# Kernel optimization log

Hardware: AMD Instinct MI355X
Metric: run time of the kernel (lower is better)

Reference implementation:

```python
import jax, jax.numpy as jnp
import numpy as np

B, S, HID = 2, 2048, 2048
H, KVH, D = 32, 8, 64          # query heads, kv heads, head_dim
G = H // KVH                    # GQA group size (num_key_value_groups)
ROT = 32                        # head_dim * partial_rotary_factor
THETA = 10000.0
NEG = -1e9


def setup_inputs() -> dict:
    key = jax.random.key(0)
    ks = jax.random.split(key, 5)
    hidden_states = jax.random.normal(ks[0], (B, S, HID), jnp.float32) * 0.02
    Wq = jax.random.normal(ks[1], (H * D, HID), jnp.float32) * 0.02
    Wk = jax.random.normal(ks[2], (KVH * D, HID), jnp.float32) * 0.02
    Wv = jax.random.normal(ks[3], (KVH * D, HID), jnp.float32) * 0.02
    Wo = jax.random.normal(ks[4], (HID, H * D), jnp.float32) * 0.02
    # rotary embeddings over the partial rotary dims
    inv_freq = 1.0 / (THETA ** (jnp.arange(0, ROT, 2, dtype=jnp.float32) / ROT))
    freqs = jnp.arange(S, dtype=jnp.float32)[:, None] * inv_freq[None, :]  # [S, ROT/2]
    emb = jnp.concatenate([freqs, freqs], axis=-1)                         # [S, ROT]
    cos = jnp.broadcast_to(jnp.cos(emb)[None], (B, S, ROT)).astype(jnp.float32)
    sin = jnp.broadcast_to(jnp.sin(emb)[None], (B, S, ROT)).astype(jnp.float32)
    # HF-style additive causal mask [1, 1, S, S]
    causal = jnp.tril(jnp.ones((S, S), dtype=bool))
    attention_mask = jnp.where(causal, 0.0, NEG).astype(jnp.float32)[None, None]
    return {"hidden_states": hidden_states, "cos": cos, "sin": sin,
            "attention_mask": attention_mask, "Wq": Wq, "Wk": Wk, "Wv": Wv, "Wo": Wo}


def _rotate_half(x):
    half = x.shape[-1] // 2
    return jnp.concatenate([-x[..., half:], x[..., :half]], axis=-1)


def _apply_partial_rope(x, cos, sin):
    # x: [B, h, S, D]; cos/sin: [B, 1, S, ROT]
    xr, xp = x[..., :ROT], x[..., ROT:]
    xr = xr * cos + _rotate_half(xr) * sin
    return jnp.concatenate([xr, xp], axis=-1)


def reference(hidden_states, cos, sin, attention_mask, Wq, Wk, Wv, Wo):
    bsz, q_len, _ = hidden_states.shape
    q = (hidden_states @ Wq.T).reshape(bsz, q_len, H, D).transpose(0, 2, 1, 3)    # [B,H,S,D]
    k = (hidden_states @ Wk.T).reshape(bsz, q_len, KVH, D).transpose(0, 2, 1, 3)  # [B,KVH,S,D]
    v = (hidden_states @ Wv.T).reshape(bsz, q_len, KVH, D).transpose(0, 2, 1, 3)
    cos_e, sin_e = cos[:, None], sin[:, None]  # unsqueeze_dim=1
    q = _apply_partial_rope(q, cos_e, sin_e)
    k = _apply_partial_rope(k, cos_e, sin_e)
    # GQA: group q heads instead of materializing repeat_kv (same math)
    qg = q.reshape(bsz, KVH, G, q_len, D)
    scores = jnp.einsum('bkgsd,bktd->bkgst', qg, k) / jnp.sqrt(jnp.float32(D))
    scores = scores + attention_mask[:, :, None, :, :q_len]  # [B,KVH,G,S,S]
    attn = jax.nn.softmax(scores.astype(jnp.float32), axis=-1).astype(q.dtype)
    out = jnp.einsum('bkgst,bktd->bkgsd', attn, v)
    out = out.reshape(bsz, H, q_len, D).transpose(0, 2, 1, 3).reshape(bsz, q_len, H * D)
    return out @ Wo.T
```

## Files before the change

kernel.cpp:

```cpp
#include <hip/hip_runtime.h>
#include <hip/hip_bf16.h>

#define BATCH 2
#define SEQ 2048
#define HID 2048
#define NH 32
#define NKVH 8
#define HD 64
#define GQ 4
#define ROT 32

typedef __attribute__((ext_vector_type(8))) short bf16x8;
typedef __attribute__((ext_vector_type(8))) unsigned short u16x8;
typedef __attribute__((ext_vector_type(4))) float f32x4;
typedef unsigned int u32;
typedef unsigned short u16;

#define MFMA_BF16(A, B, C) __builtin_amdgcn_mfma_f32_16x16x32_bf16(A, B, C, 0, 0, 0)

#define QSCALE 0.180336880111120f

__device__ __forceinline__ void gload_lds16(const void* g, void* l) {
    __builtin_amdgcn_global_load_lds(
        (const __attribute__((address_space(1))) unsigned int*)g,
        (__attribute__((address_space(3))) unsigned int*)l, 16, 0, 0);
}

__device__ __forceinline__ u16 f2b(float x) {
    union { __hip_bfloat16 h; u16 u; } cv;
    cv.h = __float2bfloat16(x);
    return cv.u;
}
__device__ __forceinline__ u32 pack2r(float lo, float hi) {
    u32 a = __builtin_bit_cast(u32, lo) + 0x8000u;
    u32 b = __builtin_bit_cast(u32, hi) + 0x8000u;
    return __builtin_amdgcn_perm(b, a, 0x07060302u);
}

__global__ __launch_bounds__(256) void cast_all(
    const float* __restrict__ hs, const float* __restrict__ Wq,
    const float* __restrict__ Wk, const float* __restrict__ Wv,
    const float* __restrict__ Wo, u16* __restrict__ d_hs, u16* __restrict__ d_Wq,
    u16* __restrict__ d_Wk, u16* __restrict__ d_Wv, u16* __restrict__ d_Wo) {
    const int bx = blockIdx.x;
    const float* s;
    u16* d;
    int off;
    if (bx < 4096) { s = hs; d = d_hs; off = bx; }
    else if (bx < 6144) { s = Wq; d = d_Wq; off = bx - 4096; }
    else if (bx < 6656) { s = Wk; d = d_Wk; off = bx - 6144; }
    else if (bx < 7168) { s = Wv; d = d_Wv; off = bx - 6656; }
    else { s = Wo; d = d_Wo; off = bx - 7168; }
    const size_t i = (size_t)off * 2048 + threadIdx.x * 8;
    const float4 a = *(const float4*)&s[i];
    const float4 b = *(const float4*)&s[i + 4];
    u16x8 v;
    v[0] = f2b(a.x); v[1] = f2b(a.y); v[2] = f2b(a.z); v[3] = f2b(a.w);
    v[4] = f2b(b.x); v[5] = f2b(b.y); v[6] = f2b(b.z); v[7] = f2b(b.w);
    *(u16x8*)&d[i] = v;
}

__global__ __launch_bounds__(256) void qkv_gemm(
    const u16* __restrict__ A, const u16* __restrict__ Wq,
    const u16* __restrict__ Wk, const u16* __restrict__ Wv,
    u16* __restrict__ Qb, u16* __restrict__ Kb, u16* __restrict__ Vt,
    const float* __restrict__ cosp, const float* __restrict__ sinp) {
    const int x = blockIdx.x;
    int mode, n0;
    const u16* __restrict__ W;
    if (x < 16)      { mode = 0; W = Wq; n0 = x * 128; }
    else if (x < 20) { mode = 1; W = Wk; n0 = (x - 16) * 128; }
    else             { mode = 2; W = Wv; n0 = (x - 20) * 128; }

    __shared__ __align__(16) u16 As[128 * 32];
    __shared__ __align__(16) u16 Ws[128 * 32];
    const int tid = threadIdx.x;
    const int lane = tid & 63, wave = tid >> 6;
    const int ar = lane & 15, quad = lane >> 4;
    const int m0 = blockIdx.y * 128;
    const int wm = (wave >> 1) * 64, wn = (wave & 1) * 64;

    f32x4 acc[4][4] = {};

    for (int k0 = 0; k0 < HID; k0 += 32) {
#pragma unroll
        for (int it = 0; it < 2; ++it) {
            const int ci = it * 256 + tid;
            const int row = ci >> 2, kcl = ci & 3;
            const int kcg = kcl ^ ((row >> 1) & 3);
            gload_lds16(&A[(size_t)(m0 + row) * HID + k0 + kcg * 8], &As[ci * 8]);
            gload_lds16(&W[(size_t)(n0 + row) * HID + k0 + kcg * 8], &Ws[ci * 8]);
        }
        __syncthreads();
        bf16x8 af[4], bf[4];
#pragma unroll
        for (int t = 0; t < 4; ++t) {
            const int ra = wm + t * 16 + ar;
            af[t] = *(const bf16x8*)&As[ra * 32 + (quad ^ ((ra >> 1) & 3)) * 8];
            const int rb = wn + t * 16 + ar;
            bf[t] = *(const bf16x8*)&Ws[rb * 32 + (quad ^ ((rb >> 1) & 3)) * 8];
        }
#pragma unroll
        for (int mt = 0; mt < 4; ++mt)
#pragma unroll
            for (int nt = 0; nt < 4; ++nt)
                acc[mt][nt] = MFMA_BF16(af[mt], bf[nt], acc[mt][nt]);
        __syncthreads();
    }

    if (mode < 2) {
        const float SC = (mode == 0) ? QSCALE : 1.0f;
        u16* __restrict__ C = (mode == 0) ? Qb : Kb;
        const int N = (mode == 0) ? 2048 : 512;
#pragma unroll
        for (int mt = 0; mt < 4; ++mt) {
            const int r0 = m0 + wm + mt * 16 + quad * 4;
#pragma unroll
            for (int r = 0; r < 4; ++r) {
                const int t = r0 + r;
                const float* cp = &cosp[(size_t)t * ROT];
                const float* sp = &sinp[(size_t)t * ROT];
                const float c0 = cp[ar], s0 = sp[ar];
                const float c1 = cp[ar + 16], s1 = sp[ar + 16];
                const float x0 = acc[mt][0][r], x1 = acc[mt][1][r];
                u16* crow = &C[(size_t)t * N + n0 + wn];
                crow[ar]      = f2b((x0 * c0 - x1 * s0) * SC);
                crow[ar + 16] = f2b((x1 * c1 + x0 * s1) * SC);
                crow[ar + 32] = f2b(acc[mt][2][r] * SC);
                crow[ar + 48] = f2b(acc[mt][3][r] * SC);
            }
        }
    } else {
#pragma unroll
        for (int mt = 0; mt < 4; ++mt) {
            const int r0 = m0 + wm + mt * 16 + quad * 4;
            const int bb = r0 >> 11;
            const int s = r0 & 2047;
            const int ca = (s >> 2) & 7;
            const int cl = ((ca & 3) << 1) | (ca >> 2);
            const int spos = (s & ~31) + cl * 4;
#pragma unroll
            for (int nt = 0; nt < 4; ++nt) {
                const int c = n0 + wn + nt * 16 + ar;
                const int kvh = c >> 6, d = c & 63;
                ushort4 v;
                v.x = f2b(acc[mt][nt][0]); v.y = f2b(acc[mt][nt][1]);
                v.z = f2b(acc[mt][nt][2]); v.w = f2b(acc[mt][nt][3]);
                *(ushort4*)&Vt[((size_t)(bb * NKVH + kvh) * HD + d) * SEQ + spos] = v;
            }
        }
    }
}

__global__ __launch_bounds__(256) void gemm_bt(const u16* __restrict__ A,
                                               const u16* __restrict__ W,
                                               float* __restrict__ C,
                                               int M, int N, int K) {
    __shared__ __align__(16) u16 As[128 * 32];
    __shared__ __align__(16) u16 Ws[128 * 32];
    const int tid = threadIdx.x;
    const int lane = tid & 63, wave = tid >> 6;
    const int ar = lane & 15, quad = lane >> 4;
    const int m0 = blockIdx.y * 128, n0 = blockIdx.x * 128;
    const int wm = (wave >> 1) * 64, wn = (wave & 1) * 64;

    f32x4 acc[4][4] = {};

    for (int k0 = 0; k0 < K; k0 += 32) {
#pragma unroll
        for (int it = 0; it < 2; ++it) {
            const int ci = it * 256 + tid;
            const int row = ci >> 2, kcl = ci & 3;
            const int kcg = kcl ^ ((row >> 1) & 3);
            gload_lds16(&A[(size_t)(m0 + row) * K + k0 + kcg * 8], &As[ci * 8]);
            gload_lds16(&W[(size_t)(n0 + row) * K + k0 + kcg * 8], &Ws[ci * 8]);
        }
        __syncthreads();
        bf16x8 af[4], bf[4];
#pragma unroll
        for (int t = 0; t < 4; ++t) {
            const int ra = wm + t * 16 + ar;
            af[t] = *(const bf16x8*)&As[ra * 32 + (quad ^ ((ra >> 1) & 3)) * 8];
            const int rb = wn + t * 16 + ar;
            bf[t] = *(const bf16x8*)&Ws[rb * 32 + (quad ^ ((rb >> 1) & 3)) * 8];
        }
#pragma unroll
        for (int mt = 0; mt < 4; ++mt)
#pragma unroll
            for (int nt = 0; nt < 4; ++nt)
                acc[mt][nt] = MFMA_BF16(af[mt], bf[nt], acc[mt][nt]);
        __syncthreads();
    }

#pragma unroll
    for (int mt = 0; mt < 4; ++mt) {
        const int r0 = m0 + wm + mt * 16 + quad * 4;
#pragma unroll
        for (int nt = 0; nt < 4; ++nt) {
            const int c = n0 + wn + nt * 16 + ar;
#pragma unroll
            for (int r = 0; r < 4; ++r)
                C[(size_t)(r0 + r) * N + c] = acc[mt][nt][r];
        }
    }
}

__global__ __launch_bounds__(256, 2) void flash_attn_mfma(
    const u16* __restrict__ Qg, const u16* __restrict__ Kg,
    const u16* __restrict__ Vtg, u16* __restrict__ AO) {
    const int p = blockIdx.x, h = blockIdx.y, b = blockIdx.z;
    const int kvh = h / GQ;
    const int tid = threadIdx.x;
    const int lane = tid & 63, w = tid >> 6;
    const int n = lane & 15, quad = lane >> 4;

    __shared__ __align__(16) u16 Qs[128 * 64];
    __shared__ __align__(16) u16 Ks[2 * 64 * 64];
    __shared__ __align__(16) u16 Vts[2 * 64 * 64];

    for (int ph = 0; ph < 2; ++ph) {
        const int bq = ph ? (15 - p) : p;
        const int q0 = bq * 128;

#pragma unroll
        for (int it = 0; it < 4; ++it) {
            const int ci = it * 256 + tid;
            const int row = ci >> 3, kcg = (ci & 7) ^ (row & 7);
            gload_lds16(&Qg[(size_t)((b * SEQ + q0 + row) * NH + h) * HD + kcg * 8],
                        &Qs[ci * 8]);
        }
#pragma unroll
        for (int it = 0; it < 2; ++it) {
            const int ci = it * 256 + tid;
            const int row = ci >> 3, kcg = (ci & 7) ^ (row & 7);
            gload_lds16(&Kg[(size_t)((b * SEQ + row) * NKVH + kvh) * HD + kcg * 8],
                        &Ks[ci * 8]);
            gload_lds16(&Vtg[(size_t)((b * NKVH + kvh) * HD + row) * SEQ + kcg * 8],
                        &Vts[ci * 8]);
        }
        __syncthreads();

        bf16x8 Qf[2][2];
#pragma unroll
        for (int t = 0; t < 2; ++t)
#pragma unroll
            for (int kh = 0; kh < 2; ++kh) {
                const int qrow = w * 32 + t * 16 + n;
                const int c = (kh * 4 + quad) ^ (qrow & 7);
                Qf[t][kh] = *(const bf16x8*)&Qs[qrow * 64 + c * 8];
            }

        f32x4 O[2][4] = {};
        float lsum[2] = {0.f, 0.f};

        const int ktmax = 2 * bq + 1;
        for (int kt = 0; kt <= ktmax; ++kt) {
            const int cur = kt & 1;
            if (kt < ktmax) {
                const int base = (cur ^ 1) * 4096;
#pragma unroll
                for (int it = 0; it < 2; ++it) {
                    const int ci = it * 256 + tid;
                    const int row = ci >> 3, kcg = (ci & 7) ^ (row & 7);
                    gload_lds16(&Kg[(size_t)((b * SEQ + (kt + 1) * 64 + row) * NKVH + kvh) * HD + kcg * 8],
                                &Ks[base + ci * 8]);
                    gload_lds16(&Vtg[(size_t)((b * NKVH + kvh) * HD + row) * SEQ + (kt + 1) * 64 + kcg * 8],
                                &Vts[base + ci * 8]);
                }
            }
            const u16* Kl = &Ks[cur * 4096];
            const u16* Vl = &Vts[cur * 4096];

            f32x4 sc[2][4] = {};
#pragma unroll
            for (int kh = 0; kh < 2; ++kh)
#pragma unroll
                for (int k4 = 0; k4 < 4; ++k4) {
                    const int krow = k4 * 16 + n;
                    const int c = (kh * 4 + quad) ^ (krow & 7);
                    const bf16x8 Kf = *(const bf16x8*)&Kl[krow * 64 + c * 8];
                    sc[0][k4] = MFMA_BF16(Kf, Qf[0][kh], sc[0][k4]);
                    sc[1][k4] = MFMA_BF16(Kf, Qf[1][kh], sc[1][k4]);
                }

            const bool masked = (kt >= 2 * bq);
            bf16x8 Pf[2][2];
#pragma unroll
            for (int t = 0; t < 2; ++t) {
                const int qg = q0 + w * 32 + t * 16 + n;
                if (masked) {
#pragma unroll
                    for (int k4 = 0; k4 < 4; ++k4)
#pragma unroll
                        for (int r = 0; r < 4; ++r)
                            if (kt * 64 + k4 * 16 + quad * 4 + r > qg)
                                sc[t][k4][r] = -1e30f;
                }
                float sk[4];
#pragma unroll
                for (int k4 = 0; k4 < 4; ++k4) {
                    const float e0 = exp2f(sc[t][k4][0]);
                    const float e1 = exp2f(sc[t][k4][1]);
                    const float e2 = exp2f(sc[t][k4][2]);
                    const float e3 = exp2f(sc[t][k4][3]);
                    sc[t][k4][0] = e0; sc[t][k4][1] = e1;
                    sc[t][k4][2] = e2; sc[t][k4][3] = e3;
                    sk[k4] = (e0 + e1) + (e2 + e3);
                }
                lsum[t] += (sk[0] + sk[1]) + (sk[2] + sk[3]);
#pragma unroll
                for (int kb = 0; kb < 2; ++kb) {
                    union { u32 uw[4]; bf16x8 v; } cv;
#pragma unroll
                    for (int a = 0; a < 2; ++a) {
                        cv.uw[a * 2 + 0] = pack2r(sc[t][2 * kb + a][0], sc[t][2 * kb + a][1]);
                        cv.uw[a * 2 + 1] = pack2r(sc[t][2 * kb + a][2], sc[t][2 * kb + a][3]);
                    }
                    Pf[t][kb] = cv.v;
                }
            }

#pragma unroll
            for (int kb = 0; kb < 2; ++kb)
#pragma unroll
                for (int dt = 0; dt < 4; ++dt) {
                    const int drow = dt * 16 + n;
                    const int c = (kb * 4 + quad) ^ (drow & 7);
                    const bf16x8 Vf = *(const bf16x8*)&Vl[drow * 64 + c * 8];
                    O[0][dt] = MFMA_BF16(Vf, Pf[0][kb], O[0][dt]);
                    O[1][dt] = MFMA_BF16(Vf, Pf[1][kb], O[1][dt]);
                }
            __syncthreads();
        }

#pragma unroll
        for (int t = 0; t < 2; ++t) {
            float rs = lsum[t];
            rs += __shfl_xor(rs, 16, 64);
            rs += __shfl_xor(rs, 32, 64);
            const int qg = q0 + w * 32 + t * 16 + n;
            const float inv = 1.f / rs;
#pragma unroll
            for (int dt = 0; dt < 4; ++dt) {
                u32 v2[2];
                v2[0] = pack2r(O[t][dt][0] * inv, O[t][dt][1] * inv);
                v2[1] = pack2r(O[t][dt][2] * inv, O[t][dt][3] * inv);
                *(u32*)&AO[(size_t)((b * SEQ + qg) * NH + h) * HD + dt * 16 + quad * 4] = v2[0];
                *(u32*)&AO[(size_t)((b * SEQ + qg) * NH + h) * HD + dt * 16 + quad * 4 + 2] = v2[1];
            }
        }
    }
}

extern "C" void kernel_launch(void* const* d_in, const int* in_sizes, int n_in,
                              void* d_out, int out_size, void* d_ws,
                              size_t ws_size, hipStream_t stream) {
    const float* hs = (const float*)d_in[0];
    const float* cosp = (const float*)d_in[1];
    const float* sinp = (const float*)d_in[2];
    const float* Wq = (const float*)d_in[4];
    const float* Wk = (const float*)d_in[5];
    const float* Wv = (const float*)d_in[6];
    const float* Wo = (const float*)d_in[7];
    float* out = (float*)d_out;

    u16* ws = (u16*)d_ws;
    u16* hs_bf = ws;
    u16* Wq_bf = hs_bf + (size_t)4096 * 2048;
    u16* Wk_bf = Wq_bf + (size_t)2048 * 2048;
    u16* Wv_bf = Wk_bf + (size_t)512 * 2048;
    u16* Wo_bf = Wv_bf + (size_t)512 * 2048;
    u16* Qb = Wo_bf + (size_t)2048 * 2048;
    u16* Kb = Qb + (size_t)4096 * 2048;
    u16* Vt = Kb + (size_t)4096 * 512;
    u16* AO = hs_bf;

    cast_all<<<dim3(9216), 256, 0, stream>>>(hs, Wq, Wk, Wv, Wo, hs_bf, Wq_bf,
                                             Wk_bf, Wv_bf, Wo_bf);

    qkv_gemm<<<dim3(24, 32), 256, 0, stream>>>(hs_bf, Wq_bf, Wk_bf, Wv_bf, Qb,
                                               Kb, Vt, cosp, sinp);

    flash_attn_mfma<<<dim3(8, NH, BATCH), 256, 0, stream>>>(Qb, Kb, Vt, AO);

    gemm_bt<<<dim3(16, 32), 256, 0, stream>>>(AO, Wo_bf, out, 4096, 2048, 2048);
}
```

Baseline: 337.6 us.

## Remap GEMM blocks per XCD and transpose MFMA operands for vectorized epilogue stores

Both GEMM kernels now use a 1D grid whose block index is remapped so that the blocks sharing a weight column-tile land on the same XCD, aiming to improve L2 reuse of weight tiles. The MFMA operands are swapped for the Q/K and output GEMMs so each lane holds four consecutive columns, which lets the epilogues use packed 8-byte and 16-byte stores and float4 cos/sin loads instead of scalar stores. The V path and the attention output store also switch to packed uint2 writes. The mapping depends on the round-robin assignment of blocks to XCDs and on grid sizes that divide evenly.

```diff
diff --git a/kernel.cpp b/kernel.cpp
--- a/kernel.cpp
+++ b/kernel.cpp
@@ -65,7 +65,11 @@
     const u16* __restrict__ Wk, const u16* __restrict__ Wv,
     u16* __restrict__ Qb, u16* __restrict__ Kb, u16* __restrict__ Vt,
     const float* __restrict__ cosp, const float* __restrict__ sinp) {
-    const int x = blockIdx.x;
+    const int bid = blockIdx.x;
+    const int xcd = bid & 7, loc = bid >> 3;
+    const int x = xcd * 3 + (loc % 3);
+    const int m0 = (loc / 3) * 128;
+
     int mode, n0;
     const u16* __restrict__ W;
     if (x < 16)      { mode = 0; W = Wq; n0 = x * 128; }
@@ -77,7 +81,7 @@
     const int tid = threadIdx.x;
     const int lane = tid & 63, wave = tid >> 6;
     const int ar = lane & 15, quad = lane >> 4;
-    const int m0 = blockIdx.y * 128;
+    const int q4 = quad * 4;
     const int wm = (wave >> 1) * 64, wn = (wave & 1) * 64;
 
     f32x4 acc[4][4] = {};
@@ -100,11 +104,19 @@
             const int rb = wn + t * 16 + ar;
             bf[t] = *(const bf16x8*)&Ws[rb * 32 + (quad ^ ((rb >> 1) & 3)) * 8];
         }
-#pragma unroll
-        for (int mt = 0; mt < 4; ++mt)
-#pragma unroll
-            for (int nt = 0; nt < 4; ++nt)
-                acc[mt][nt] = MFMA_BF16(af[mt], bf[nt], acc[mt][nt]);
+        if (mode < 2) {
+#pragma unroll
+            for (int mt = 0; mt < 4; ++mt)
+#pragma unroll
+                for (int nt = 0; nt < 4; ++nt)
+                    acc[mt][nt] = MFMA_BF16(bf[nt], af[mt], acc[mt][nt]);
+        } else {
+#pragma unroll
+            for (int mt = 0; mt < 4; ++mt)
+#pragma unroll
+                for (int nt = 0; nt < 4; ++nt)
+                    acc[mt][nt] = MFMA_BF16(af[mt], bf[nt], acc[mt][nt]);
+        }
         __syncthreads();
     }
 
@@ -114,26 +126,39 @@
         const int N = (mode == 0) ? 2048 : 512;
 #pragma unroll
         for (int mt = 0; mt < 4; ++mt) {
-            const int r0 = m0 + wm + mt * 16 + quad * 4;
+            const int t = m0 + wm + mt * 16 + ar;
+            const float4 c0 = *(const float4*)&cosp[(size_t)t * ROT + q4];
+            const float4 s0 = *(const float4*)&sinp[(size_t)t * ROT + q4];
+            const float4 c1 = *(const float4*)&cosp[(size_t)t * ROT + 16 + q4];
+            const float4 s1 = *(const float4*)&sinp[(size_t)t * ROT + 16 + q4];
+            u16* crow = &C[(size_t)t * N + n0 + wn];
+            const f32x4 x0 = acc[mt][0], x1 = acc[mt][1];
+            const float cr0[4] = {c0.x, c0.y, c0.z, c0.w};
+            const float sr0[4] = {s0.x, s0.y, s0.z, s0.w};
+            const float cr1[4] = {c1.x, c1.y, c1.z, c1.w};
+            const float sr1[4] = {s1.x, s1.y, s1.z, s1.w};
+            float o0[4], o1[4];
 #pragma unroll
             for (int r = 0; r < 4; ++r) {
-                const int t = r0 + r;
-                const float* cp = &cosp[(size_t)t * ROT];
-                const float* sp = &sinp[(size_t)t * ROT];
-                const float c0 = cp[ar], s0 = sp[ar];
-                const float c1 = cp[ar + 16], s1 = sp[ar + 16];
-                const float x0 = acc[mt][0][r], x1 = acc[mt][1][r];
-                u16* crow = &C[(size_t)t * N + n0 + wn];
-                crow[ar]      = f2b((x0 * c0 - x1 * s0) * SC);
-                crow[ar + 16] = f2b((x1 * c1 + x0 * s1) * SC);
-                crow[ar + 32] = f2b(acc[mt][2][r] * SC);
-                crow[ar + 48] = f2b(acc[mt][3][r] * SC);
-            }
+                o0[r] = (x0[r] * cr0[r] - x1[r] * sr0[r]) * SC;
+                o1[r] = (x1[r] * cr1[r] + x0[r] * sr1[r]) * SC;
+            }
+            uint2 v;
+            v.x = pack2r(o0[0], o0[1]); v.y = pack2r(o0[2], o0[3]);
+            *(uint2*)&crow[q4] = v;
+            v.x = pack2r(o1[0], o1[1]); v.y = pack2r(o1[2], o1[3]);
+            *(uint2*)&crow[16 + q4] = v;
+            v.x = pack2r(acc[mt][2][0] * SC, acc[mt][2][1] * SC);
+            v.y = pack2r(acc[mt][2][2] * SC, acc[mt][2][3] * SC);
+            *(uint2*)&crow[32 + q4] = v;
+            v.x = pack2r(acc[mt][3][0] * SC, acc[mt][3][1] * SC);
+            v.y = pack2r(acc[mt][3][2] * SC, acc[mt][3][3] * SC);
+            *(uint2*)&crow[48 + q4] = v;
         }
     } else {
 #pragma unroll
         for (int mt = 0; mt < 4; ++mt) {
-            const int r0 = m0 + wm + mt * 16 + quad * 4;
+            const int r0 = m0 + wm + mt * 16 + q4;
             const int bb = r0 >> 11;
             const int s = r0 & 2047;
             const int ca = (s >> 2) & 7;
@@ -143,10 +168,10 @@
             for (int nt = 0; nt < 4; ++nt) {
                 const int c = n0 + wn + nt * 16 + ar;
                 const int kvh = c >> 6, d = c & 63;
-                ushort4 v;
-                v.x = f2b(acc[mt][nt][0]); v.y = f2b(acc[mt][nt][1]);
-                v.z = f2b(acc[mt][nt][2]); v.w = f2b(acc[mt][nt][3]);
-                *(ushort4*)&Vt[((size_t)(bb * NKVH + kvh) * HD + d) * SEQ + spos] = v;
+                uint2 v;
+                v.x = pack2r(acc[mt][nt][0], acc[mt][nt][1]);
+                v.y = pack2r(acc[mt][nt][2], acc[mt][nt][3]);
+                *(uint2*)&Vt[((size_t)(bb * NKVH + kvh) * HD + d) * SEQ + spos] = v;
             }
         }
     }
@@ -156,12 +181,17 @@
                                                const u16* __restrict__ W,
                                                float* __restrict__ C,
                                                int M, int N, int K) {
+    const int bid = blockIdx.x;
+    const int xcd = bid & 7, loc = bid >> 3;
+    const int n0 = (xcd * 2 + (loc & 1)) * 128;
+    const int m0 = (loc >> 1) * 128;
+
     __shared__ __align__(16) u16 As[128 * 32];
     __shared__ __align__(16) u16 Ws[128 * 32];
     const int tid = threadIdx.x;
     const int lane = tid & 63, wave = tid >> 6;
     const int ar = lane & 15, quad = lane >> 4;
-    const int m0 = blockIdx.y * 128, n0 = blockIdx.x * 128;
+    const int q4 = quad * 4;
     const int wm = (wave >> 1) * 64, wn = (wave & 1) * 64;
 
     f32x4 acc[4][4] = {};
@@ -188,19 +218,17 @@
         for (int mt = 0; mt < 4; ++mt)
 #pragma unroll
             for (int nt = 0; nt < 4; ++nt)
-                acc[mt][nt] = MFMA_BF16(af[mt], bf[nt], acc[mt][nt]);
+                acc[mt][nt] = MFMA_BF16(bf[nt], af[mt], acc[mt][nt]);
         __syncthreads();
     }
 
 #pragma unroll
     for (int mt = 0; mt < 4; ++mt) {
-        const int r0 = m0 + wm + mt * 16 + quad * 4;
+        const int t = m0 + wm + mt * 16 + ar;
 #pragma unroll
         for (int nt = 0; nt < 4; ++nt) {
-            const int c = n0 + wn + nt * 16 + ar;
-#pragma unroll
-            for (int r = 0; r < 4; ++r)
-                C[(size_t)(r0 + r) * N + c] = acc[mt][nt][r];
+            float4 v = {acc[mt][nt][0], acc[mt][nt][1], acc[mt][nt][2], acc[mt][nt][3]};
+            *(float4*)&C[(size_t)t * N + n0 + wn + nt * 16 + q4] = v;
         }
     }
 }
@@ -342,11 +370,10 @@
             const float inv = 1.f / rs;
 #pragma unroll
             for (int dt = 0; dt < 4; ++dt) {
-                u32 v2[2];
-                v2[0] = pack2r(O[t][dt][0] * inv, O[t][dt][1] * inv);
-                v2[1] = pack2r(O[t][dt][2] * inv, O[t][dt][3] * inv);
-                *(u32*)&AO[(size_t)((b * SEQ + qg) * NH + h) * HD + dt * 16 + quad * 4] = v2[0];
-                *(u32*)&AO[(size_t)((b * SEQ + qg) * NH + h) * HD + dt * 16 + quad * 4 + 2] = v2[1];
+                uint2 v2;
+                v2.x = pack2r(O[t][dt][0] * inv, O[t][dt][1] * inv);
+                v2.y = pack2r(O[t][dt][2] * inv, O[t][dt][3] * inv);
+                *(uint2*)&AO[(size_t)((b * SEQ + qg) * NH + h) * HD + dt * 16 + quad * 4] = v2;
             }
         }
     }
@@ -378,10 +405,10 @@
     cast_all<<<dim3(9216), 256, 0, stream>>>(hs, Wq, Wk, Wv, Wo, hs_bf, Wq_bf,
                                              Wk_bf, Wv_bf, Wo_bf);
 
-    qkv_gemm<<<dim3(24, 32), 256, 0, stream>>>(hs_bf, Wq_bf, Wk_bf, Wv_bf, Qb,
-                                               Kb, Vt, cosp, sinp);
+    qkv_gemm<<<dim3(768), 256, 0, stream>>>(hs_bf, Wq_bf, Wk_bf, Wv_bf, Qb,
+                                            Kb, Vt, cosp, sinp);
 
     flash_attn_mfma<<<dim3(8, NH, BATCH), 256, 0, stream>>>(Qb, Kb, Vt, AO);
 
-    gemm_bt<<<dim3(16, 32), 256, 0, stream>>>(AO, Wo_bf, out, 4096, 2048, 2048);
-}
+    gemm_bt<<<dim3(512), 256, 0, stream>>>(AO, Wo_bf, out, 4096, 2048, 2048);
+}
```

Result: no change. 341.3 us (+1.1%).
